# Kernel optimization log

Hardware: AMD Instinct MI355X
Metric: run time of the kernel (lower is better)

Reference implementation:

```python
import jax, jax.numpy as jnp
import numpy as np
import math

LOG2PI = math.log(2.0 * math.pi)
ALPHA, BETA, GAMMA = 1.0, 4.0, 1.0  # coefficients (mi, tc, dw_kl)


def gaussian_log_density(samples, mean, log_var):
    inv_sigma = jnp.exp(-log_var)
    tmp = samples - mean
    return -0.5 * (tmp * tmp * inv_sigma + log_var + LOG2PI)


def log_importance_weight_matrix(batch_size, dataset_size):
    # Faithful port of the TF/beta-tcvae MSS importance weights.
    N = float(dataset_size)
    M = batch_size - 1
    strat_weight = (N - M) / (N * M)
    W = jnp.full((batch_size, batch_size), 1.0 / M, dtype=jnp.float32)
    W = W.at[:, 0].set(1.0 / N)
    W = W.at[:, 1].set(strat_weight)
    W = W.at[M - 1, 0].set(strat_weight)
    return jnp.log(W)


def setup_inputs() -> dict:
    key = jax.random.key(0)
    k1, k2, k3, k4, k5 = jax.random.split(key, 5)
    B, D, F = 2048, 16, 512
    return {
        "x": jax.random.normal(k1, (B, F), dtype=jnp.float32),
        "reconstruction": jax.random.normal(k2, (B, F), dtype=jnp.float32),
        "mu": jax.random.normal(k3, (B, D), dtype=jnp.float32),
        "log_var": jax.random.normal(k4, (B, D), dtype=jnp.float32) * 0.5,
        "z": jax.random.normal(k5, (B, D), dtype=jnp.float32),
        "size_dataset": 100000,
    }


def reference(x, reconstruction, mu, log_var, z, size_dataset):
    B = z.shape[0]
    # reconstruction loss: mean over batch of per-sample MAE == global mean abs error
    recon_loss = jnp.mean(jnp.abs(x - reconstruction))

    # log q(z|x): [B]
    log_q_zx = jnp.sum(gaussian_log_density(z, mu, log_var), axis=-1)

    # pairwise densities: [B, B, D]  (z_i under q(.|x_j))
    log_qz_prob = gaussian_log_density(z[:, None, :], mu[None, :, :], log_var[None, :, :])

    # log p(z): note the original passes ones_like(z) as log_var (faithful quirk)
    log_prior = jnp.sum(
        gaussian_log_density(z, jnp.zeros_like(z), jnp.ones_like(z)), axis=-1
    )

    # MSS importance weights [B, B]
    logiw = log_importance_weight_matrix(B, size_dataset)

    # log q(z): logsumexp over batch of joint densities + weights
    log_qz = jax.nn.logsumexp(jnp.sum(log_qz_prob, axis=2) + logiw, axis=1)  # [B]

    # log prod_d q(z_d): dimension-wise logsumexp then sum over dims
    log_qz_product = jnp.sum(
        jax.nn.logsumexp(log_qz_prob + logiw[:, :, None], axis=1), axis=1
    )  # [B]

    mutual_info_loss = jnp.mean(log_q_zx - log_qz)
    tc_loss = jnp.mean(log_qz - log_qz_product)
    dimension_wise_kl = jnp.mean(log_qz_product - log_prior)

    total_loss = (
        recon_loss
        + ALPHA * mutual_info_loss
        + BETA * tc_loss
        + GAMMA * dimension_wise_kl
    )
    return total_loss
```

## Files before the change

kernel.cpp:

```cpp
#include <hip/hip_runtime.h>
#include <math.h>

#define LOG2PI_F 1.8378770664093453f
#define LOG2E_F  1.4426950408889634f
#define LN2_F    0.6931471805599453f
#define EXP_NEG1 0.36787944117144233f

#define ROWF 52
#define JSP  32
#define JCH  64

__device__ __forceinline__ float exp2_(float x) { return __builtin_amdgcn_exp2f(x); }
__device__ __forceinline__ float log2_(float x) { return __builtin_amdgcn_logf(x); }


__global__ __launch_bounds__(256) void k_front(const float* __restrict__ mu,
                                               const float* __restrict__ lv,
                                               const float* __restrict__ z,
                                               const int* __restrict__ nds,
                                               const float4* __restrict__ x,
                                               const float4* __restrict__ r,
                                               float* __restrict__ ws,
                                               int B, int n4, int prepBlocks,
                                               int reconBlocks) {
    const int bx = blockIdx.x;
    if (bx == 0 && threadIdx.x == 0) *(int*)(ws + 960) = 0;

    __shared__ float ra[4], rb[4];
    int lane = threadIdx.x & 63, wv = threadIdx.x >> 6;

    if (bx < prepBlocks) {
        float* AC = ws + 1024;
        float* prepPart = ws + 512;
        int idx = bx * 256 + threadIdx.x;
        int j = idx >> 4, d = idx & 15;
        float m = mu[idx], l = lv[idx], zz = z[idx];
        float is = __expf(-l);
        float a = -0.5f * LOG2E_F * is;
        float ec = -0.5f * LOG2E_F * (l + LOG2PI_F);

        float Nf = (float)(*nds);
        float Mf = (float)(B - 1);
        float strat = (Nf - Mf) / (Nf * Mf);
        float w = (j == 0) ? (1.0f / Nf) : ((j == 1) ? strat : (1.0f / Mf));

        float* row = AC + (size_t)j * ROWF;
        row[d] = a;
        row[16 + d] = m;
        row[32 + d] = w * exp2_(ec);
        float es = ec;
        es += __shfl_xor(es, 1); es += __shfl_xor(es, 2);
        es += __shfl_xor(es, 4); es += __shfl_xor(es, 8);
        if (d == 0) row[48] = w * exp2_(es);

        float t = zz - m;
        float ga = -0.5f * (fmaf(t * t, is, l) + LOG2PI_F);
        float gb = -0.5f * (fmaf(zz * zz, EXP_NEG1, 1.0f) + LOG2PI_F);
        #pragma unroll
        for (int off = 32; off > 0; off >>= 1) { ga += __shfl_down(ga, off); gb += __shfl_down(gb, off); }
        if (lane == 0) { ra[wv] = ga; rb[wv] = gb; }
        __syncthreads();
        if (threadIdx.x == 0) {
            prepPart[bx * 2 + 0] = ra[0] + ra[1] + ra[2] + ra[3];
            prepPart[bx * 2 + 1] = rb[0] + rb[1] + rb[2] + rb[3];
        }
    } else {
        float* reconPart = ws;
        int rbk = bx - prepBlocks;
        float s = 0.0f;
        for (int idx = rbk * 256 + threadIdx.x; idx < n4; idx += reconBlocks * 256) {
            float4 a = x[idx], b = r[idx];
            s += fabsf(a.x - b.x) + fabsf(a.y - b.y) + fabsf(a.z - b.z) + fabsf(a.w - b.w);
        }
        #pragma unroll
        for (int off = 32; off > 0; off >>= 1) s += __shfl_down(s, off);
        if (lane == 0) ra[wv] = s;
        __syncthreads();
        if (threadIdx.x == 0) reconPart[rbk] = ra[0] + ra[1] + ra[2] + ra[3];
    }
}

__global__ __launch_bounds__(256) void k_pair(const float* __restrict__ AC,
                                              const float* __restrict__ zg,
                                              float* __restrict__ Racc, int B) {
    __shared__ float sAC[JCH * ROWF];
    __shared__ float red[4][16][17];

    const int il = threadIdx.x & 15;
    const int jg = threadIdx.x >> 4;
    const int i  = blockIdx.x * 16 + il;

    {
        const float4* g = (const float4*)(AC + (size_t)blockIdx.y * JCH * ROWF);
        float4* s4 = (float4*)sAC;
        for (int u = threadIdx.x; u < (JCH * ROWF) / 4; u += 256) s4[u] = g[u];
    }

    float v[16];
    {
        const float4* zp = (const float4*)(zg + (size_t)i * 16);
        float4 a0 = zp[0], a1 = zp[1], a2 = zp[2], a3 = zp[3];
        v[0]=a0.x; v[1]=a0.y; v[2]=a0.z; v[3]=a0.w;
        v[4]=a1.x; v[5]=a1.y; v[6]=a1.z; v[7]=a1.w;
        v[8]=a2.x; v[9]=a2.y; v[10]=a2.z; v[11]=a2.w;
        v[12]=a3.x; v[13]=a3.y; v[14]=a3.z; v[15]=a3.w;
    }

    float sd[16];
    #pragma unroll
    for (int d = 0; d < 16; ++d) sd[d] = 0.0f;
    float stot = 0.0f;

    __syncthreads();

    #pragma unroll
    for (int k = 0; k < 4; ++k) {
        const float* rp = sAC + (jg + 16 * k) * ROWF;
        float P = rp[48];
        float s2 = 0.0f;
        #pragma unroll
        for (int dq = 0; dq < 4; ++dq) {
            float4 aq = *(const float4*)(rp + dq * 4);
            float4 mq = *(const float4*)(rp + 16 + dq * 4);
            float4 cq = *(const float4*)(rp + 32 + dq * 4);
            const int d0 = dq * 4;
            float t0 = v[d0+0] - mq.x; float e0 = (aq.x * t0) * t0;
            float t1 = v[d0+1] - mq.y; float e1 = (aq.y * t1) * t1;
            float t2 = v[d0+2] - mq.z; float e2 = (aq.z * t2) * t2;
            float t3 = v[d0+3] - mq.w; float e3 = (aq.w * t3) * t3;
            s2 += (e0 + e1) + (e2 + e3);
            sd[d0+0] = fmaf(cq.x, exp2_(e0), sd[d0+0]);
            sd[d0+1] = fmaf(cq.y, exp2_(e1), sd[d0+1]);
            sd[d0+2] = fmaf(cq.z, exp2_(e2), sd[d0+2]);
            sd[d0+3] = fmaf(cq.w, exp2_(e3), sd[d0+3]);
        }
        stot = fmaf(P, exp2_(s2), stot);
    }

    #pragma unroll
    for (int msk = 16; msk <= 32; msk <<= 1) {
        stot += __shfl_xor(stot, msk);
        #pragma unroll
        for (int d = 0; d < 16; ++d) sd[d] += __shfl_xor(sd[d], msk);
    }
    int lane = threadIdx.x & 63, wv = threadIdx.x >> 6;
    if (lane < 16) {
        red[wv][lane][0] = stot;
        #pragma unroll
        for (int d = 0; d < 16; ++d) red[wv][lane][1 + d] = sd[d];
    }
    __syncthreads();
    for (int t = threadIdx.x; t < 16 * 17; t += 256) {
        int il2 = t & 15, c = t >> 4;
        float s = red[0][il2][c] + red[1][il2][c] + red[2][il2][c] + red[3][il2][c];
        Racc[((size_t)blockIdx.y * 17 + c) * B + blockIdx.x * 16 + il2] = s;
    }
}

__global__ __launch_bounds__(256) void k_logs(float* __restrict__ ws,
                                              const float* __restrict__ zg,
                                              const int* __restrict__ nds,
                                              float* __restrict__ out,
                                              int B, float invBF, float invB) {
    float* reconPart = ws;
    float* prepPart  = ws + 512;
    float* logsPart  = ws + 768;
    int*   counter   = (int*)(ws + 960);
    const float* AC  = ws + 1024;
    const float* Racc = AC + (size_t)B * ROWF;

    int fl = blockIdx.x * 256 + threadIdx.x;
    int c  = fl / B;
    int i  = fl - c * B;

    float s = 0.0f;
    #pragma unroll 8
    for (int sl = 0; sl < JSP; ++sl)
        s += Racc[((size_t)sl * 17 + c) * B + i];

    if (i == B - 2) {
        const float* vv = zg + (size_t)(B - 2) * 16;
        float Nf = (float)(*nds);
        float Mf = (float)(B - 1);
        float dwN = (Nf - 2.0f * Mf) / Mf;
        if (c == 0) {
            float s2 = 0.0f;
            #pragma unroll
            for (int d = 0; d < 16; ++d) {
                float t = vv[d] - AC[16 + d];
                s2 += (AC[d] * t) * t;
            }
            s += dwN * AC[48] * exp2_(s2);
        } else {
            int d = c - 1;
            float t = vv[d] - AC[16 + d];
            s += dwN * AC[32 + d] * exp2_((AC[d] * t) * t);
        }
    }

    float contrib = ((c == 0) ? 3.0f : -3.0f) * log2_(s) * LN2_F;
    #pragma unroll
    for (int off = 32; off > 0; off >>= 1) contrib += __shfl_down(contrib, off);
    __shared__ float ra[4];
    __shared__ int lastFlag;
    int lane = threadIdx.x & 63, wv = threadIdx.x >> 6;
    if (lane == 0) ra[wv] = contrib;
    __syncthreads();
    if (threadIdx.x == 0) {
        __hip_atomic_store(&logsPart[blockIdx.x], ra[0] + ra[1] + ra[2] + ra[3],
                           __ATOMIC_RELEASE, __HIP_MEMORY_SCOPE_AGENT);
        int old = __hip_atomic_fetch_add(counter, 1, __ATOMIC_ACQ_REL, __HIP_MEMORY_SCOPE_AGENT);
        lastFlag = (old == (int)gridDim.x - 1);
    }
    __syncthreads();

    if (lastFlag) {
        int t = threadIdx.x;
        float rec = 0.0f, X = 0.0f, P = 0.0f, QD = 0.0f;
        for (int k = t; k < 512; k += 256) rec += reconPart[k];
        if (t < 128) { X = prepPart[2 * t]; P = prepPart[2 * t + 1]; }
        if (t < (int)gridDim.x)
            QD = __hip_atomic_load(&logsPart[t], __ATOMIC_ACQUIRE, __HIP_MEMORY_SCOPE_AGENT);
        #pragma unroll
        for (int off = 32; off > 0; off >>= 1) {
            rec += __shfl_down(rec, off);
            X   += __shfl_down(X, off);
            P   += __shfl_down(P, off);
            QD  += __shfl_down(QD, off);
        }
        __shared__ float fin[4][4];
        int ln = t & 63, w2 = t >> 6;
        if (ln == 0) { fin[w2][0] = rec; fin[w2][1] = X; fin[w2][2] = P; fin[w2][3] = QD; }
        __syncthreads();
        if (t == 0) {
            float R  = fin[0][0] + fin[1][0] + fin[2][0] + fin[3][0];
            float Xs = fin[0][1] + fin[1][1] + fin[2][1] + fin[3][1];
            float Ps = fin[0][2] + fin[1][2] + fin[2][2] + fin[3][2];
            float Qs = fin[0][3] + fin[1][3] + fin[2][3] + fin[3][3];
            out[0] = R * invBF + (Xs - Ps + Qs) * invB;
        }
    }
}

extern "C" void kernel_launch(void* const* d_in, const int* in_sizes, int n_in,
                              void* d_out, int out_size, void* d_ws, size_t ws_size,
                              hipStream_t stream) {
    const float* x   = (const float*)d_in[0];
    const float* rec = (const float*)d_in[1];
    const float* mu  = (const float*)d_in[2];
    const float* lv  = (const float*)d_in[3];
    const float* z   = (const float*)d_in[4];
    const int*   nds = (const int*)d_in[5];

    const int BD = in_sizes[2];
    const int B  = BD / 16;
    const int BF = in_sizes[0];
    const int n4 = BF / 4;

    float* ws   = (float*)d_ws;
    float* AC   = ws + 1024;
    float* Racc = AC + (size_t)B * ROWF;

    const int prepBlocks  = BD / 256;
    const int reconBlocks = 512;

    k_front<<<prepBlocks + reconBlocks, 256, 0, stream>>>(
        mu, lv, z, nds, (const float4*)x, (const float4*)rec, ws,
        B, n4, prepBlocks, reconBlocks);
    dim3 gp(B / 16, JSP);
    k_pair<<<gp, 256, 0, stream>>>(AC, z, Racc, B);
    k_logs<<<(17 * B) / 256, 256, 0, stream>>>(ws, z, nds, (float*)d_out,
                                               B, 1.0f / (float)BF, 1.0f / (float)B);
}
```

Before: 102.9 us.

## Fuse pairwise, log, and recon reductions into one kernel with full-row j sweep

Replaces the three-kernel pipeline with a small prep kernel and one fused kernel. Each 1024-thread block owns 8 rows of i and sweeps all j in 512-row LDS chunks, so the per-i sums are finished inside the block. This removes the Racc partial buffer round-trip and the separate log kernel. The reconstruction MAE and the per-sample log densities are folded into the same block and reduced through a last-block atomic. The cost is only 256 large blocks, each holding about 104KB of LDS, which gives low occupancy and a serial loop over j per block.

```diff
diff --git a/kernel.cpp b/kernel.cpp
--- a/kernel.cpp
+++ b/kernel.cpp
@@ -6,96 +6,86 @@
 #define LN2_F    0.6931471805599453f
 #define EXP_NEG1 0.36787944117144233f
 
-#define ROWF 52
-#define JSP  32
-#define JCH  64
+#define ROWF   52
+#define CHROWS 512
+#define ITI    8
+#define NT     1024
 
 __device__ __forceinline__ float exp2_(float x) { return __builtin_amdgcn_exp2f(x); }
 __device__ __forceinline__ float log2_(float x) { return __builtin_amdgcn_logf(x); }
 
 
-__global__ __launch_bounds__(256) void k_front(const float* __restrict__ mu,
-                                               const float* __restrict__ lv,
-                                               const float* __restrict__ z,
-                                               const int* __restrict__ nds,
-                                               const float4* __restrict__ x,
-                                               const float4* __restrict__ r,
-                                               float* __restrict__ ws,
-                                               int B, int n4, int prepBlocks,
-                                               int reconBlocks) {
+__global__ __launch_bounds__(256) void k_prep(const float* __restrict__ mu,
+                                              const float* __restrict__ lv,
+                                              const int* __restrict__ nds,
+                                              float* __restrict__ ws, int B) {
+    if (blockIdx.x == 0 && threadIdx.x == 0) *(int*)(ws + 256) = 0;
+    float* AC = ws + 1024;
+    int idx = blockIdx.x * 256 + threadIdx.x;
+    int j = idx >> 4, d = idx & 15;
+    float m = mu[idx], l = lv[idx];
+    float a = -0.5f * LOG2E_F * __expf(-l);
+    float ec = -0.5f * LOG2E_F * (l + LOG2PI_F);
+
+    float Nf = (float)(*nds);
+    float Mf = (float)(B - 1);
+    float strat = (Nf - Mf) / (Nf * Mf);
+    float w = (j == 0) ? (1.0f / Nf) : ((j == 1) ? strat : (1.0f / Mf));
+
+    float* row = AC + (size_t)j * ROWF;
+    row[d] = a;
+    row[16 + d] = m;
+    row[32 + d] = w * exp2_(ec);
+    float es = ec;
+    es += __shfl_xor(es, 1); es += __shfl_xor(es, 2);
+    es += __shfl_xor(es, 4); es += __shfl_xor(es, 8);
+    if (d == 0) row[48] = w * exp2_(es);
+}
+
+__global__ __launch_bounds__(1024) void k_all(const float* __restrict__ ws_ac,
+                                              const float* __restrict__ zg,
+                                              const float* __restrict__ mu,
+                                              const float* __restrict__ lv,
+                                              const float4* __restrict__ x,
+                                              const float4* __restrict__ r,
+                                              const int* __restrict__ nds,
+                                              float* __restrict__ wsPart,
+                                              int* __restrict__ counter,
+                                              float* __restrict__ out,
+                                              int B, int n4,
+                                              float invBF, float invB,
+                                              int nblocks, int pb, int pil) {
+    __shared__ float lds[CHROWS * ROWF];
+    __shared__ float fin[16];
+    __shared__ int lastFlag;
+
+    const float* AC = ws_ac + 1024;
+    const int t = threadIdx.x;
     const int bx = blockIdx.x;
-    if (bx == 0 && threadIdx.x == 0) *(int*)(ws + 960) = 0;
-
-    __shared__ float ra[4], rb[4];
-    int lane = threadIdx.x & 63, wv = threadIdx.x >> 6;
-
-    if (bx < prepBlocks) {
-        float* AC = ws + 1024;
-        float* prepPart = ws + 512;
-        int idx = bx * 256 + threadIdx.x;
-        int j = idx >> 4, d = idx & 15;
-        float m = mu[idx], l = lv[idx], zz = z[idx];
-        float is = __expf(-l);
-        float a = -0.5f * LOG2E_F * is;
-        float ec = -0.5f * LOG2E_F * (l + LOG2PI_F);
-
-        float Nf = (float)(*nds);
-        float Mf = (float)(B - 1);
-        float strat = (Nf - Mf) / (Nf * Mf);
-        float w = (j == 0) ? (1.0f / Nf) : ((j == 1) ? strat : (1.0f / Mf));
-
-        float* row = AC + (size_t)j * ROWF;
-        row[d] = a;
-        row[16 + d] = m;
-        row[32 + d] = w * exp2_(ec);
-        float es = ec;
-        es += __shfl_xor(es, 1); es += __shfl_xor(es, 2);
-        es += __shfl_xor(es, 4); es += __shfl_xor(es, 8);
-        if (d == 0) row[48] = w * exp2_(es);
-
-        float t = zz - m;
-        float ga = -0.5f * (fmaf(t * t, is, l) + LOG2PI_F);
+    const int lane = t & 63, wv = t >> 6;
+    const int il = t & 7;
+    const int jgrp = t >> 3;
+    const int i = bx * ITI + il;
+
+    float rec_s = 0.0f;
+    {
+        int per = (n4 + nblocks - 1) / nblocks;
+        int lo = bx * per, hi = min(lo + per, n4);
+        for (int u = lo + t; u < hi; u += NT) {
+            float4 a = x[u], b = r[u];
+            rec_s += fabsf(a.x - b.x) + fabsf(a.y - b.y) + fabsf(a.z - b.z) + fabsf(a.w - b.w);
+        }
+    }
+    float gab = 0.0f;
+    if (t < ITI * 16) {
+        int iw = t >> 4, d = t & 15;
+        int idx = (bx * ITI + iw) * 16 + d;
+        float m = mu[idx], l = lv[idx], zz = zg[idx];
+        float tt = zz - m;
+        float ga = -0.5f * (fmaf(tt * tt, __expf(-l), l) + LOG2PI_F);
         float gb = -0.5f * (fmaf(zz * zz, EXP_NEG1, 1.0f) + LOG2PI_F);
-        #pragma unroll
-        for (int off = 32; off > 0; off >>= 1) { ga += __shfl_down(ga, off); gb += __shfl_down(gb, off); }
-        if (lane == 0) { ra[wv] = ga; rb[wv] = gb; }
-        __syncthreads();
-        if (threadIdx.x == 0) {
-            prepPart[bx * 2 + 0] = ra[0] + ra[1] + ra[2] + ra[3];
-            prepPart[bx * 2 + 1] = rb[0] + rb[1] + rb[2] + rb[3];
-        }
-    } else {
-        float* reconPart = ws;
-        int rbk = bx - prepBlocks;
-        float s = 0.0f;
-        for (int idx = rbk * 256 + threadIdx.x; idx < n4; idx += reconBlocks * 256) {
-            float4 a = x[idx], b = r[idx];
-            s += fabsf(a.x - b.x) + fabsf(a.y - b.y) + fabsf(a.z - b.z) + fabsf(a.w - b.w);
-        }
-        #pragma unroll
-        for (int off = 32; off > 0; off >>= 1) s += __shfl_down(s, off);
-        if (lane == 0) ra[wv] = s;
-        __syncthreads();
-        if (threadIdx.x == 0) reconPart[rbk] = ra[0] + ra[1] + ra[2] + ra[3];
-    }
-}
-
-__global__ __launch_bounds__(256) void k_pair(const float* __restrict__ AC,
-                                              const float* __restrict__ zg,
-                                              float* __restrict__ Racc, int B) {
-    __shared__ float sAC[JCH * ROWF];
-    __shared__ float red[4][16][17];
-
-    const int il = threadIdx.x & 15;
-    const int jg = threadIdx.x >> 4;
-    const int i  = blockIdx.x * 16 + il;
-
-    {
-        const float4* g = (const float4*)(AC + (size_t)blockIdx.y * JCH * ROWF);
-        float4* s4 = (float4*)sAC;
-        for (int u = threadIdx.x; u < (JCH * ROWF) / 4; u += 256) s4[u] = g[u];
-    }
-
+        gab = ga - gb;
+    }
     float v[16];
     {
         const float4* zp = (const float4*)(zg + (size_t)i * 16);
@@ -111,133 +101,113 @@
     for (int d = 0; d < 16; ++d) sd[d] = 0.0f;
     float stot = 0.0f;
 
-    __syncthreads();
-
-    #pragma unroll
-    for (int k = 0; k < 4; ++k) {
-        const float* rp = sAC + (jg + 16 * k) * ROWF;
-        float P = rp[48];
-        float s2 = 0.0f;
-        #pragma unroll
-        for (int dq = 0; dq < 4; ++dq) {
-            float4 aq = *(const float4*)(rp + dq * 4);
-            float4 mq = *(const float4*)(rp + 16 + dq * 4);
-            float4 cq = *(const float4*)(rp + 32 + dq * 4);
-            const int d0 = dq * 4;
-            float t0 = v[d0+0] - mq.x; float e0 = (aq.x * t0) * t0;
-            float t1 = v[d0+1] - mq.y; float e1 = (aq.y * t1) * t1;
-            float t2 = v[d0+2] - mq.z; float e2 = (aq.z * t2) * t2;
-            float t3 = v[d0+3] - mq.w; float e3 = (aq.w * t3) * t3;
-            s2 += (e0 + e1) + (e2 + e3);
-            sd[d0+0] = fmaf(cq.x, exp2_(e0), sd[d0+0]);
-            sd[d0+1] = fmaf(cq.y, exp2_(e1), sd[d0+1]);
-            sd[d0+2] = fmaf(cq.z, exp2_(e2), sd[d0+2]);
-            sd[d0+3] = fmaf(cq.w, exp2_(e3), sd[d0+3]);
-        }
-        stot = fmaf(P, exp2_(s2), stot);
-    }
-
-    #pragma unroll
-    for (int msk = 16; msk <= 32; msk <<= 1) {
-        stot += __shfl_xor(stot, msk);
-        #pragma unroll
-        for (int d = 0; d < 16; ++d) sd[d] += __shfl_xor(sd[d], msk);
-    }
-    int lane = threadIdx.x & 63, wv = threadIdx.x >> 6;
-    if (lane < 16) {
-        red[wv][lane][0] = stot;
-        #pragma unroll
-        for (int d = 0; d < 16; ++d) red[wv][lane][1 + d] = sd[d];
-    }
-    __syncthreads();
-    for (int t = threadIdx.x; t < 16 * 17; t += 256) {
-        int il2 = t & 15, c = t >> 4;
-        float s = red[0][il2][c] + red[1][il2][c] + red[2][il2][c] + red[3][il2][c];
-        Racc[((size_t)blockIdx.y * 17 + c) * B + blockIdx.x * 16 + il2] = s;
-    }
-}
-
-__global__ __launch_bounds__(256) void k_logs(float* __restrict__ ws,
-                                              const float* __restrict__ zg,
-                                              const int* __restrict__ nds,
-                                              float* __restrict__ out,
-                                              int B, float invBF, float invB) {
-    float* reconPart = ws;
-    float* prepPart  = ws + 512;
-    float* logsPart  = ws + 768;
-    int*   counter   = (int*)(ws + 960);
-    const float* AC  = ws + 1024;
-    const float* Racc = AC + (size_t)B * ROWF;
-
-    int fl = blockIdx.x * 256 + threadIdx.x;
-    int c  = fl / B;
-    int i  = fl - c * B;
-
-    float s = 0.0f;
-    #pragma unroll 8
-    for (int sl = 0; sl < JSP; ++sl)
-        s += Racc[((size_t)sl * 17 + c) * B + i];
-
-    if (i == B - 2) {
-        const float* vv = zg + (size_t)(B - 2) * 16;
-        float Nf = (float)(*nds);
-        float Mf = (float)(B - 1);
-        float dwN = (Nf - 2.0f * Mf) / Mf;
-        if (c == 0) {
+    const int nch = B / CHROWS;
+    for (int c = 0; c < nch; ++c) {
+        __syncthreads();
+        {
+            const float4* g = (const float4*)(AC + (size_t)c * CHROWS * ROWF);
+            float4* s4 = (float4*)lds;
+            for (int u = t; u < (CHROWS * ROWF) / 4; u += NT) s4[u] = g[u];
+        }
+        __syncthreads();
+        #pragma unroll
+        for (int k = 0; k < CHROWS / 128; ++k) {
+            const float* rp = lds + (jgrp + 128 * k) * ROWF;
+            float P = rp[48];
             float s2 = 0.0f;
             #pragma unroll
-            for (int d = 0; d < 16; ++d) {
-                float t = vv[d] - AC[16 + d];
-                s2 += (AC[d] * t) * t;
+            for (int dq = 0; dq < 4; ++dq) {
+                float4 aq = *(const float4*)(rp + dq * 4);
+                float4 mq = *(const float4*)(rp + 16 + dq * 4);
+                float4 cq = *(const float4*)(rp + 32 + dq * 4);
+                const int d0 = dq * 4;
+                float t0 = v[d0+0] - mq.x; float e0 = (aq.x * t0) * t0;
+                float t1 = v[d0+1] - mq.y; float e1 = (aq.y * t1) * t1;
+                float t2 = v[d0+2] - mq.z; float e2 = (aq.z * t2) * t2;
+                float t3 = v[d0+3] - mq.w; float e3 = (aq.w * t3) * t3;
+                s2 += (e0 + e1) + (e2 + e3);
+                sd[d0+0] = fmaf(cq.x, exp2_(e0), sd[d0+0]);
+                sd[d0+1] = fmaf(cq.y, exp2_(e1), sd[d0+1]);
+                sd[d0+2] = fmaf(cq.z, exp2_(e2), sd[d0+2]);
+                sd[d0+3] = fmaf(cq.w, exp2_(e3), sd[d0+3]);
             }
-            s += dwN * AC[48] * exp2_(s2);
-        } else {
-            int d = c - 1;
-            float t = vv[d] - AC[16 + d];
-            s += dwN * AC[32 + d] * exp2_((AC[d] * t) * t);
-        }
-    }
-
-    float contrib = ((c == 0) ? 3.0f : -3.0f) * log2_(s) * LN2_F;
+            stot = fmaf(P, exp2_(s2), stot);
+        }
+    }
+
     #pragma unroll
-    for (int off = 32; off > 0; off >>= 1) contrib += __shfl_down(contrib, off);
-    __shared__ float ra[4];
-    __shared__ int lastFlag;
-    int lane = threadIdx.x & 63, wv = threadIdx.x >> 6;
-    if (lane == 0) ra[wv] = contrib;
-    __syncthreads();
-    if (threadIdx.x == 0) {
-        __hip_atomic_store(&logsPart[blockIdx.x], ra[0] + ra[1] + ra[2] + ra[3],
-                           __ATOMIC_RELEASE, __HIP_MEMORY_SCOPE_AGENT);
+    for (int m = 8; m <= 32; m <<= 1) {
+        stot += __shfl_xor(stot, m);
+        #pragma unroll
+        for (int d = 0; d < 16; ++d) sd[d] += __shfl_xor(sd[d], m);
+    }
+    __syncthreads();
+    if (lane < 8) {
+        float* wp = lds + (wv * 8 + lane) * 17;
+        wp[0] = stot;
+        #pragma unroll
+        for (int d = 0; d < 16; ++d) wp[1 + d] = sd[d];
+    }
+    __syncthreads();
+
+    float contrib = 0.0f;
+    if (t < ITI * 17) {
+        int il2 = t / 17, cc = t % 17;
+        float S = 0.0f;
+        #pragma unroll
+        for (int w = 0; w < 16; ++w) S += lds[w * 136 + t];
+
+        if (bx == pb && il2 == pil) {
+            const float* vv = zg + (size_t)(B - 2) * 16;
+            float Nf = (float)(*nds);
+            float Mf = (float)(B - 1);
+            float dwN = (Nf - 2.0f * Mf) / Mf;
+            if (cc == 0) {
+                float s2 = 0.0f;
+                #pragma unroll
+                for (int d = 0; d < 16; ++d) {
+                    float tt = vv[d] - AC[16 + d];
+                    s2 += (AC[d] * tt) * tt;
+                }
+                S += dwN * AC[48] * exp2_(s2);
+            } else {
+                int d = cc - 1;
+                float tt = vv[d] - AC[16 + d];
+                S += dwN * AC[32 + d] * exp2_((AC[d] * tt) * tt);
+            }
+        }
+        contrib = ((cc == 0) ? 3.0f : -3.0f) * log2_(S) * LN2_F;
+    }
+
+    float phi = rec_s * invBF + (gab + contrib) * invB;
+    #pragma unroll
+    for (int off = 32; off > 0; off >>= 1) phi += __shfl_down(phi, off);
+    if (lane == 0) fin[wv] = phi;
+    __syncthreads();
+    if (t == 0) {
+        float s = 0.0f;
+        #pragma unroll
+        for (int w = 0; w < 16; ++w) s += fin[w];
+        __hip_atomic_store(&wsPart[bx], s, __ATOMIC_RELEASE, __HIP_MEMORY_SCOPE_AGENT);
         int old = __hip_atomic_fetch_add(counter, 1, __ATOMIC_ACQ_REL, __HIP_MEMORY_SCOPE_AGENT);
-        lastFlag = (old == (int)gridDim.x - 1);
+        lastFlag = (old == nblocks - 1);
     }
     __syncthreads();
 
     if (lastFlag) {
-        int t = threadIdx.x;
-        float rec = 0.0f, X = 0.0f, P = 0.0f, QD = 0.0f;
-        for (int k = t; k < 512; k += 256) rec += reconPart[k];
-        if (t < 128) { X = prepPart[2 * t]; P = prepPart[2 * t + 1]; }
-        if (t < (int)gridDim.x)
-            QD = __hip_atomic_load(&logsPart[t], __ATOMIC_ACQUIRE, __HIP_MEMORY_SCOPE_AGENT);
-        #pragma unroll
-        for (int off = 32; off > 0; off >>= 1) {
-            rec += __shfl_down(rec, off);
-            X   += __shfl_down(X, off);
-            P   += __shfl_down(P, off);
-            QD  += __shfl_down(QD, off);
-        }
-        __shared__ float fin[4][4];
-        int ln = t & 63, w2 = t >> 6;
-        if (ln == 0) { fin[w2][0] = rec; fin[w2][1] = X; fin[w2][2] = P; fin[w2][3] = QD; }
+        float q = 0.0f;
+        if (t < nblocks)
+            q = __hip_atomic_load(&wsPart[t], __ATOMIC_ACQUIRE, __HIP_MEMORY_SCOPE_AGENT);
+        #pragma unroll
+        for (int off = 32; off > 0; off >>= 1) q += __shfl_down(q, off);
+        __syncthreads();
+        if (lane == 0) fin[wv] = q;
         __syncthreads();
         if (t == 0) {
-            float R  = fin[0][0] + fin[1][0] + fin[2][0] + fin[3][0];
-            float Xs = fin[0][1] + fin[1][1] + fin[2][1] + fin[3][1];
-            float Ps = fin[0][2] + fin[1][2] + fin[2][2] + fin[3][2];
-            float Qs = fin[0][3] + fin[1][3] + fin[2][3] + fin[3][3];
-            out[0] = R * invBF + (Xs - Ps + Qs) * invB;
+            float s = 0.0f;
+            #pragma unroll
+            for (int w = 0; w < 16; ++w) s += fin[w];
+            out[0] = s;
         }
     }
 }
@@ -257,18 +227,17 @@
     const int BF = in_sizes[0];
     const int n4 = BF / 4;
 
-    float* ws   = (float*)d_ws;
-    float* AC   = ws + 1024;
-    float* Racc = AC + (size_t)B * ROWF;
-
-    const int prepBlocks  = BD / 256;
-    const int reconBlocks = 512;
-
-    k_front<<<prepBlocks + reconBlocks, 256, 0, stream>>>(
-        mu, lv, z, nds, (const float4*)x, (const float4*)rec, ws,
-        B, n4, prepBlocks, reconBlocks);
-    dim3 gp(B / 16, JSP);
-    k_pair<<<gp, 256, 0, stream>>>(AC, z, Racc, B);
-    k_logs<<<(17 * B) / 256, 256, 0, stream>>>(ws, z, nds, (float*)d_out,
-                                               B, 1.0f / (float)BF, 1.0f / (float)B);
+    float* ws      = (float*)d_ws;
+    float* wsPart  = ws;
+    int*   counter = (int*)(ws + 256);
+    const int nblocks = B / ITI;
+    const int pb  = (B - 2) / ITI;
+    const int pil = (B - 2) % ITI;
+
+    k_prep<<<BD / 256, 256, 0, stream>>>(mu, lv, nds, ws, B);
+    k_all<<<nblocks, NT, 0, stream>>>(ws, z, mu, lv,
+                                      (const float4*)x, (const float4*)rec, nds,
+                                      wsPart, counter, (float*)d_out,
+                                      B, n4, 1.0f / (float)BF, 1.0f / (float)B,
+                                      nblocks, pb, pil);
 }
```

Measured after the change: 103.8 us. No clear change (+0.9%).
